# Kernel tuning notes

Hardware: AMD Instinct MI355X
Metric: run time of the kernel (lower is better)

Reference implementation:

```python
import jax, jax.numpy as jnp
import numpy as np

DIM = 3
SIGMA_MIN = 0.05
NORM_EPS = 1e-10
DEG2RAD = np.pi / 180.0


def setup_inputs() -> dict:
    key = jax.random.key(0)
    kF, = jax.random.split(key, 1)
    B = 4_000_000
    F = jax.random.normal(kF, (B, 3, 3), dtype=jnp.float32)
    return {
        "F": F,
        "youngs_modulus_log": jnp.asarray(np.log(2_000_000.0), dtype=jnp.float32),
        "poissons_ratio": jnp.asarray(0.4, dtype=jnp.float32),
        "friction_angle": jnp.asarray(25.0, dtype=jnp.float32),
        "cohesion": jnp.asarray(0.0, dtype=jnp.float32),
    }


def reference(F, youngs_modulus_log, poissons_ratio, friction_angle, cohesion):
    E = jnp.exp(youngs_modulus_log)
    sin_phi = jnp.sin(friction_angle * DEG2RAD)
    alpha = jnp.sqrt(2.0 / 3.0) * 2.0 * sin_phi / (3.0 - sin_phi)
    mu = E / (2.0 * (1.0 + poissons_ratio))
    la = E * poissons_ratio / ((1.0 + poissons_ratio) * (1.0 - 2.0 * poissons_ratio))

    # Batched 3x3 SVD: U (B,3,3), sigma (B,3), Vh (B,3,3)
    U, sigma, Vh = jnp.linalg.svd(F, full_matrices=False)

    sigma = jnp.maximum(sigma, SIGMA_MIN)
    eps = jnp.log(sigma)                                   # log strain (B,3)
    trace = eps.sum(axis=1, keepdims=True)                 # (B,1)
    eps_hat = eps - trace / DIM                            # deviatoric part
    eps_hat_norm = jnp.maximum(
        jnp.linalg.norm(eps_hat, axis=1, keepdims=True), NORM_EPS)
    shifted_trace = trace - cohesion * DIM
    cond_yield = shifted_trace < 0.0                       # (B,1)
    delta_gamma = eps_hat_norm + (DIM * la + 2.0 * mu) / (2.0 * mu) * shifted_trace * alpha
    compress_eps = eps - jnp.maximum(delta_gamma, 0.0) / eps_hat_norm * eps_hat
    expand_eps = jnp.ones_like(eps) * cohesion
    eps_corrected = jnp.where(cond_yield, compress_eps, expand_eps)

    # F_corrected = U @ diag(exp(eps_corrected)) @ Vh
    F_corrected = jnp.einsum('bij,bj,bjk->bik', U, jnp.exp(eps_corrected), Vh)
    return F_corrected
```

## Files before the change

### kernel.cpp

```cpp
#include <hip/hip_runtime.h>
#include <math.h>

#define BLOCK 256
#define EPT   2
#define EPB   (BLOCK * EPT)
#define FPB   (EPB * 9)
#define F4PB  (FPB / 4)

__device__ __forceinline__ float frcp(float x)   { return __builtin_amdgcn_rcpf(x); }
__device__ __forceinline__ float frsq(float x)   { return __builtin_amdgcn_rsqf(x); }
__device__ __forceinline__ float fsqrt_r(float x){ return __builtin_amdgcn_sqrtf(x); }

__device__ __forceinline__ float acos_fast(float x) {
    float ax = fabsf(x);
    float p = fmaf(ax, -0.0187293f, 0.0742610f);
    p = fmaf(ax, p, -0.2121144f);
    p = fmaf(ax, p, 1.5707288f);
    float r = fsqrt_r(fmaxf(1.0f - ax, 0.0f)) * p;
    return (x < 0.0f) ? (3.14159265358979f - r) : r;
}

__device__ __forceinline__ void best_cross(
    float r0x, float r0y, float r0z,
    float r1x, float r1y, float r1z,
    float r2x, float r2y, float r2z,
    float& bx, float& by, float& bz, float& bn)
{
    float c0x = fmaf(r0y,r1z, -r0z*r1y);
    float c0y = fmaf(r0z,r1x, -r0x*r1z);
    float c0z = fmaf(r0x,r1y, -r0y*r1x);
    float c1x = fmaf(r0y,r2z, -r0z*r2y);
    float c1y = fmaf(r0z,r2x, -r0x*r2z);
    float c1z = fmaf(r0x,r2y, -r0y*r2x);
    float c2x = fmaf(r1y,r2z, -r1z*r2y);
    float c2y = fmaf(r1z,r2x, -r1x*r2z);
    float c2z = fmaf(r1x,r2y, -r1y*r2x);
    float n0 = fmaf(c0x,c0x, fmaf(c0y,c0y, c0z*c0z));
    float n1 = fmaf(c1x,c1x, fmaf(c1y,c1y, c1z*c1z));
    float n2 = fmaf(c2x,c2x, fmaf(c2y,c2y, c2z*c2z));
    bool b1 = n1 > n0;
    float sx = b1 ? c1x : c0x, sy = b1 ? c1y : c0y, sz = b1 ? c1z : c0z;
    float sn = b1 ? n1 : n0;
    bool b2 = n2 > sn;
    bx = b2 ? c2x : sx; by = b2 ? c2y : sy; bz = b2 ? c2z : sz;
    bn = b2 ? n2 : sn;
}

__device__ __forceinline__ void dp_solve(
    float a00, float a01, float a02,
    float a10, float a11, float a12,
    float a20, float a21, float a22,
    float coh, float ratio,
    float& r00, float& r01, float& r02,
    float& r10, float& r11, float& r12,
    float& r20, float& r21, float& r22)
{
    float s00 = fmaf(a00,a00, fmaf(a10,a10, a20*a20));
    float s11 = fmaf(a01,a01, fmaf(a11,a11, a21*a21));
    float s22 = fmaf(a02,a02, fmaf(a12,a12, a22*a22));
    float s01 = fmaf(a00,a01, fmaf(a10,a11, a20*a21));
    float s02 = fmaf(a00,a02, fmaf(a10,a12, a20*a22));
    float s12 = fmaf(a01,a02, fmaf(a11,a12, a21*a22));

    float q   = (s00 + s11 + s22) * (1.0f/3.0f);
    float b00 = s00 - q, b11 = s11 - q, b22 = s22 - q;
    float offsq = fmaf(s01,s01, fmaf(s02,s02, s12*s12));
    float p2  = fmaf(b00,b00, fmaf(b11,b11, fmaf(b22,b22, 2.0f*offsq)));
    float pp  = fsqrt_r(p2 * (1.0f/6.0f));
    float pinv = frcp(fmaxf(pp, 1e-10f));
    float det = b00*fmaf(b11,b22, -s12*s12)
              - s01*fmaf(s01,b22, -s12*s02)
              + s02*fmaf(s01,s12, -b11*s02);
    float rdet = 0.5f * det * pinv * pinv * pinv;
    rdet = fminf(fmaxf(rdet, -1.0f), 1.0f);
    float phi  = acos_fast(rdet) * (1.0f/3.0f);
    float lam0 = fmaf(2.0f*pp, __cosf(phi), q);
    float lam2 = fmaf(2.0f*pp, __cosf(phi + 2.0943951023931953f), q);

    float bx, by, bz, bn;
    best_cross(s00-lam0, s01, s02,
               s01, s11-lam0, s12,
               s02, s12, s22-lam0, bx, by, bz, bn);
    bool ok0 = bn > 1e-24f;
    float ir0 = frsq(fmaxf(bn, 1e-30f));
    float v00 = ok0 ? bx*ir0 : 1.0f;
    float v10 = ok0 ? by*ir0 : 0.0f;
    float v20 = ok0 ? bz*ir0 : 0.0f;

    best_cross(s00-lam2, s01, s02,
               s01, s11-lam2, s12,
               s02, s12, s22-lam2, bx, by, bz, bn);
    float axv = fabsf(v00), ayv = fabsf(v10), azv = fabsf(v20);
    bool xm = (axv <= ayv) && (axv <= azv);
    bool ym = (!xm) && (ayv <= azv);
    float ex = xm ? 1.0f : 0.0f;
    float ey = ym ? 1.0f : 0.0f;
    float ez = (xm || ym) ? 0.0f : 1.0f;
    float fx = fmaf(v10,ez, -v20*ey);
    float fy = fmaf(v20,ex, -v00*ez);
    float fz = fmaf(v00,ey, -v10*ex);
    bool ok2 = bn > 1e-24f;
    float wx = ok2 ? bx : fx, wy = ok2 ? by : fy, wz = ok2 ? bz : fz;
    float dp = fmaf(wx,v00, fmaf(wy,v10, wz*v20));
    wx = fmaf(-dp, v00, wx); wy = fmaf(-dp, v10, wy); wz = fmaf(-dp, v20, wz);
    float wn = fmaf(wx,wx, fmaf(wy,wy, wz*wz));
    bool okw = wn > 1e-24f;
    wx = okw ? wx : fx; wy = okw ? wy : fy; wz = okw ? wz : fz;
    wn = okw ? wn : fmaf(fx,fx, fmaf(fy,fy, fz*fz));
    float irw = frsq(fmaxf(wn, 1e-30f));
    float v02 = wx*irw, v12 = wy*irw, v22 = wz*irw;
    float v01 = fmaf(v12,v20, -v22*v10);
    float v11 = fmaf(v22,v00, -v02*v20);
    float v21 = fmaf(v02,v10, -v12*v00);

    float q0 = fmaf(a00,v00, fmaf(a01,v10, a02*v20));
    float q1 = fmaf(a10,v00, fmaf(a11,v10, a12*v20));
    float q2 = fmaf(a20,v00, fmaf(a21,v10, a22*v20));
    float m0 = fmaf(q0,q0, fmaf(q1,q1, q2*q2));
    float i0 = frsq(fmaxf(m0, 1e-30f));
    float u00 = q0*i0, u10 = q1*i0, u20 = q2*i0;

    q0 = fmaf(a00,v01, fmaf(a01,v11, a02*v21));
    q1 = fmaf(a10,v01, fmaf(a11,v11, a12*v21));
    q2 = fmaf(a20,v01, fmaf(a21,v11, a22*v21));
    float m1 = fmaf(q0,q0, fmaf(q1,q1, q2*q2));
    float i1 = frsq(fmaxf(m1, 1e-30f));
    float u01 = q0*i1, u11 = q1*i1, u21 = q2*i1;

    float u02 = fmaf(u10,u21, -u20*u11);
    float u12 = fmaf(u20,u01, -u00*u21);
    float u22 = fmaf(u00,u11, -u10*u01);

    float w0 = fmaf(a00,v02, fmaf(a01,v12, a02*v22));
    float w1 = fmaf(a10,v02, fmaf(a11,v12, a12*v22));
    float w2 = fmaf(a20,v02, fmaf(a21,v12, a22*v22));
    float s2 = fmaf(u02,w0, fmaf(u12,w1, u22*w2));

    float e0 = 0.5f * __logf(fmaxf(m0, 0.0025f));
    float e1 = 0.5f * __logf(fmaxf(m1, 0.0025f));
    float e2 = __logf(fmaxf(fabsf(s2), 0.05f));
    float tr  = e0 + e1 + e2;
    float tr3 = tr * (1.0f / 3.0f);
    float h0 = e0 - tr3, h1 = e1 - tr3, h2 = e2 - tr3;
    float hn = fsqrt_r(fmaf(h0,h0, fmaf(h1,h1, h2*h2)));
    hn = fmaxf(hn, 1e-10f);
    float st = tr - coh * 3.0f;
    float dg = hn + ratio * st;
    float sc = fmaxf(dg, 0.0f) * frcp(hn);
    bool yield = st < 0.0f;
    float ec0 = yield ? fmaf(-sc, h0, e0) : coh;
    float ec1 = yield ? fmaf(-sc, h1, e1) : coh;
    float ec2 = yield ? fmaf(-sc, h2, e2) : coh;
    float f0 = __expf(ec0);
    float f1 = __expf(ec1);
    float f2 = copysignf(__expf(ec2), s2);

    float w00 = u00*f0, w01 = u01*f1, w02 = u02*f2;
    float w10 = u10*f0, w11 = u11*f1, w12 = u12*f2;
    float w20 = u20*f0, w21 = u21*f1, w22 = u22*f2;
    r00 = fmaf(w00,v00, fmaf(w01,v01, w02*v02));
    r01 = fmaf(w00,v10, fmaf(w01,v11, w02*v12));
    r02 = fmaf(w00,v20, fmaf(w01,v21, w02*v22));
    r10 = fmaf(w10,v00, fmaf(w11,v01, w12*v02));
    r11 = fmaf(w10,v10, fmaf(w11,v11, w12*v12));
    r12 = fmaf(w10,v20, fmaf(w11,v21, w12*v22));
    r20 = fmaf(w20,v00, fmaf(w21,v01, w22*v02));
    r21 = fmaf(w20,v10, fmaf(w21,v11, w22*v12));
    r22 = fmaf(w20,v20, fmaf(w21,v21, w22*v22));
}

__global__ __launch_bounds__(BLOCK) void dp_kernel(
    const float* __restrict__ F,
    const float* __restrict__ p_yml,
    const float* __restrict__ p_nu,
    const float* __restrict__ p_fa,
    const float* __restrict__ p_coh,
    float* __restrict__ out,
    int n_elem)
{
    __shared__ float lds[FPB];
    const int t_id    = threadIdx.x;
    const int nfloats = n_elem * 9;
    const int base_f  = (int)blockIdx.x * FPB;

    #pragma unroll
    for (int j = 0; j < 5; ++j) {
        int idx = t_id + j * BLOCK;
        if (idx < F4PB) {
            int g4 = (base_f >> 2) + idx;
            int gf = g4 << 2;
            if (gf + 4 <= nfloats) {
                ((float4*)lds)[idx] = ((const float4*)F)[g4];
            } else {
                #pragma unroll
                for (int k = 0; k < 4; ++k)
                    if (gf + k < nfloats) lds[idx * 4 + k] = F[gf + k];
            }
        }
    }
    __syncthreads();

    const float yml = p_yml[0];
    const float nu  = p_nu[0];
    const float fa  = p_fa[0];
    const float coh = p_coh[0];
    const float E     = __expf(yml);
    const float sphi  = __sinf(fa * 0.017453292519943295f);
    const float alpha = 1.632993161855452f * sphi * frcp(3.0f - sphi);
    const float mu    = E * 0.5f * frcp(1.0f + nu);
    const float la    = E * nu * frcp((1.0f + nu) * (1.0f - 2.0f * nu));
    const float ratio = (3.0f * la + 2.0f * mu) * frcp(2.0f * mu) * alpha;

    const float* pA = lds + t_id * 9;
    const float* pB = lds + (t_id + BLOCK) * 9;
    float A00=pA[0], A01=pA[1], A02=pA[2];
    float A10=pA[3], A11=pA[4], A12=pA[5];
    float A20=pA[6], A21=pA[7], A22=pA[8];
    float B00=pB[0], B01=pB[1], B02=pB[2];
    float B10=pB[3], B11=pB[4], B12=pB[5];
    float B20=pB[6], B21=pB[7], B22=pB[8];

    float xa0,xa1,xa2,xa3,xa4,xa5,xa6,xa7,xa8;
    float xb0,xb1,xb2,xb3,xb4,xb5,xb6,xb7,xb8;
    dp_solve(A00,A01,A02,A10,A11,A12,A20,A21,A22, coh, ratio,
             xa0,xa1,xa2,xa3,xa4,xa5,xa6,xa7,xa8);
    dp_solve(B00,B01,B02,B10,B11,B12,B20,B21,B22, coh, ratio,
             xb0,xb1,xb2,xb3,xb4,xb5,xb6,xb7,xb8);

    {
        float* q = lds + t_id * 9;
        q[0]=xa0; q[1]=xa1; q[2]=xa2;
        q[3]=xa3; q[4]=xa4; q[5]=xa5;
        q[6]=xa6; q[7]=xa7; q[8]=xa8;
        q = lds + (t_id + BLOCK) * 9;
        q[0]=xb0; q[1]=xb1; q[2]=xb2;
        q[3]=xb3; q[4]=xb4; q[5]=xb5;
        q[6]=xb6; q[7]=xb7; q[8]=xb8;
    }
    __syncthreads();

    #pragma unroll
    for (int j = 0; j < 5; ++j) {
        int idx = t_id + j * BLOCK;
        if (idx < F4PB) {
            int g4 = (base_f >> 2) + idx;
            int gf = g4 << 2;
            if (gf + 4 <= nfloats) {
                ((float4*)out)[g4] = ((float4*)lds)[idx];
            } else {
                #pragma unroll
                for (int k = 0; k < 4; ++k)
                    if (gf + k < nfloats) out[gf + k] = lds[idx * 4 + k];
            }
        }
    }
}

extern "C" void kernel_launch(void* const* d_in, const int* in_sizes, int n_in,
                              void* d_out, int out_size, void* d_ws, size_t ws_size,
                              hipStream_t stream) {
    const float* F = (const float*)d_in[0];
    const int n_elem = in_sizes[0] / 9;
    const int grid = (n_elem + EPB - 1) / EPB;
    dp_kernel<<<grid, BLOCK, 0, stream>>>(
        F,
        (const float*)d_in[1], (const float*)d_in[2],
        (const float*)d_in[3], (const float*)d_in[4],
        (float*)d_out, n_elem);
}
```

Before: 257.2 us.

## Drop LDS staging and process one element per thread with direct global access

Replaces the cooperative float4 LDS load/store staging, two elements per thread, with each thread directly reading and writing its own 9 floats from global memory. It also sets a minimum of 8 blocks per CU in launch bounds to raise occupancy. This removes LDS traffic and barriers and lowers register pressure, but gives up vectorized coalesced transactions in favour of strided scalar accesses. It also loses the per-thread instruction-level parallelism of two independent solves.

```diff
diff --git a/kernel.cpp b/kernel.cpp
--- a/kernel.cpp
+++ b/kernel.cpp
@@ -2,10 +2,6 @@
 #include <math.h>
 
 #define BLOCK 256
-#define EPT   2
-#define EPB   (BLOCK * EPT)
-#define FPB   (EPB * 9)
-#define F4PB  (FPB / 4)
 
 __device__ __forceinline__ float frcp(float x)   { return __builtin_amdgcn_rcpf(x); }
 __device__ __forceinline__ float frsq(float x)   { return __builtin_amdgcn_rsqf(x); }
@@ -169,7 +165,7 @@
     r22 = fmaf(w20,v20, fmaf(w21,v21, w22*v22));
 }
 
-__global__ __launch_bounds__(BLOCK) void dp_kernel(
+__global__ __launch_bounds__(BLOCK, 8) void dp_kernel(
     const float* __restrict__ F,
     const float* __restrict__ p_yml,
     const float* __restrict__ p_nu,
@@ -178,27 +174,13 @@
     float* __restrict__ out,
     int n_elem)
 {
-    __shared__ float lds[FPB];
-    const int t_id    = threadIdx.x;
-    const int nfloats = n_elem * 9;
-    const int base_f  = (int)blockIdx.x * FPB;
-
-    #pragma unroll
-    for (int j = 0; j < 5; ++j) {
-        int idx = t_id + j * BLOCK;
-        if (idx < F4PB) {
-            int g4 = (base_f >> 2) + idx;
-            int gf = g4 << 2;
-            if (gf + 4 <= nfloats) {
-                ((float4*)lds)[idx] = ((const float4*)F)[g4];
-            } else {
-                #pragma unroll
-                for (int k = 0; k < 4; ++k)
-                    if (gf + k < nfloats) lds[idx * 4 + k] = F[gf + k];
-            }
-        }
-    }
-    __syncthreads();
+    const int e = (int)blockIdx.x * BLOCK + threadIdx.x;
+    if (e >= n_elem) return;
+
+    const float* p = F + e * 9;
+    float a00 = p[0], a01 = p[1], a02 = p[2];
+    float a10 = p[3], a11 = p[4], a12 = p[5];
+    float a20 = p[6], a21 = p[7], a22 = p[8];
 
     const float yml = p_yml[0];
     const float nu  = p_nu[0];
@@ -211,49 +193,14 @@
     const float la    = E * nu * frcp((1.0f + nu) * (1.0f - 2.0f * nu));
     const float ratio = (3.0f * la + 2.0f * mu) * frcp(2.0f * mu) * alpha;
 
-    const float* pA = lds + t_id * 9;
-    const float* pB = lds + (t_id + BLOCK) * 9;
-    float A00=pA[0], A01=pA[1], A02=pA[2];
-    float A10=pA[3], A11=pA[4], A12=pA[5];
-    float A20=pA[6], A21=pA[7], A22=pA[8];
-    float B00=pB[0], B01=pB[1], B02=pB[2];
-    float B10=pB[3], B11=pB[4], B12=pB[5];
-    float B20=pB[6], B21=pB[7], B22=pB[8];
-
-    float xa0,xa1,xa2,xa3,xa4,xa5,xa6,xa7,xa8;
-    float xb0,xb1,xb2,xb3,xb4,xb5,xb6,xb7,xb8;
-    dp_solve(A00,A01,A02,A10,A11,A12,A20,A21,A22, coh, ratio,
-             xa0,xa1,xa2,xa3,xa4,xa5,xa6,xa7,xa8);
-    dp_solve(B00,B01,B02,B10,B11,B12,B20,B21,B22, coh, ratio,
-             xb0,xb1,xb2,xb3,xb4,xb5,xb6,xb7,xb8);
-
-    {
-        float* q = lds + t_id * 9;
-        q[0]=xa0; q[1]=xa1; q[2]=xa2;
-        q[3]=xa3; q[4]=xa4; q[5]=xa5;
-        q[6]=xa6; q[7]=xa7; q[8]=xa8;
-        q = lds + (t_id + BLOCK) * 9;
-        q[0]=xb0; q[1]=xb1; q[2]=xb2;
-        q[3]=xb3; q[4]=xb4; q[5]=xb5;
-        q[6]=xb6; q[7]=xb7; q[8]=xb8;
-    }
-    __syncthreads();
-
-    #pragma unroll
-    for (int j = 0; j < 5; ++j) {
-        int idx = t_id + j * BLOCK;
-        if (idx < F4PB) {
-            int g4 = (base_f >> 2) + idx;
-            int gf = g4 << 2;
-            if (gf + 4 <= nfloats) {
-                ((float4*)out)[g4] = ((float4*)lds)[idx];
-            } else {
-                #pragma unroll
-                for (int k = 0; k < 4; ++k)
-                    if (gf + k < nfloats) out[gf + k] = lds[idx * 4 + k];
-            }
-        }
-    }
+    float r00,r01,r02,r10,r11,r12,r20,r21,r22;
+    dp_solve(a00,a01,a02,a10,a11,a12,a20,a21,a22, coh, ratio,
+             r00,r01,r02,r10,r11,r12,r20,r21,r22);
+
+    float* o = out + e * 9;
+    o[0]=r00; o[1]=r01; o[2]=r02;
+    o[3]=r10; o[4]=r11; o[5]=r12;
+    o[6]=r20; o[7]=r21; o[8]=r22;
 }
 
 extern "C" void kernel_launch(void* const* d_in, const int* in_sizes, int n_in,
@@ -261,7 +208,7 @@
                               hipStream_t stream) {
     const float* F = (const float*)d_in[0];
     const int n_elem = in_sizes[0] / 9;
-    const int grid = (n_elem + EPB - 1) / EPB;
+    const int grid = (n_elem + BLOCK - 1) / BLOCK;
     dp_kernel<<<grid, BLOCK, 0, stream>>>(
         F,
         (const float*)d_in[1], (const float*)d_in[2],
```

Measured after the change: 255.6 us. No clear change (-0.6%).
